# Kernel tuning notes

Measured on AMD Instinct MI355X. Metric: run time of the kernel, lower is better.

Reference implementation:

```python
import jax, jax.numpy as jnp
import numpy as np

T, E, D, F, K, CAP = 4096, 8, 1024, 4096, 2, 1024


def setup_inputs() -> dict:
    key = jax.random.key(0)
    ks = jax.random.split(key, 4)
    x = jax.random.normal(ks[0], (T, D), jnp.float32)
    # top-k routing: mask/weight consistent with a softmax router
    logits = jax.random.normal(ks[1], (T, E), jnp.float32)
    probs = jax.nn.softmax(logits, axis=-1)
    _, topi = jax.lax.top_k(probs, K)  # (T, K)
    route_mask = jnp.zeros((T, E), jnp.bool_).at[jnp.arange(T)[:, None], topi].set(True)
    route_weight = jnp.where(route_mask, probs, 0.0)
    # stacked expert MLP params (E leading axis, as ModuleGroup stacks them)
    w1 = jax.random.normal(ks[2], (E, D, F), jnp.float32) * 0.02
    b1 = jnp.zeros((E, F), jnp.float32)
    w2 = jax.random.normal(ks[3], (E, F, D), jnp.float32) * 0.02
    b2 = jnp.zeros((E, D), jnp.float32)
    return dict(x=x, route_mask=route_mask, route_weight=route_weight,
                w1=w1, b1=b1, w2=w2, b2=b2)


def _build_slots(mask_te, w_te, cap):
    # mask_te: (T,E) bool; w_te: (T,E) float (0 where unrouted)
    Tn, En = mask_te.shape
    m_et = mask_te.T                              # (E,T)
    w_et = jnp.where(m_et, w_te.T, -jnp.inf)      # unrouted -> -inf
    _, idx_top = jax.lax.top_k(w_et, cap)         # (E,C) token ids per slot
    slot = jnp.zeros((En, cap, Tn), w_te.dtype)
    slot = slot.at[jnp.arange(En)[:, None], jnp.arange(cap)[None, :], idx_top].set(1.0)
    slot = slot * m_et[:, None, :].astype(w_te.dtype)  # zero slots from -inf picks
    # NOTE: the original re-orders slots along C (a stable sort); the combine
    # einsum sums over C so the output is invariant to slot order -- skipped.
    return slot


def reference(x, route_mask, route_weight, w1, b1, w2, b2):
    w_te = jnp.where(route_mask, route_weight, 0.0)      # (T,E)
    slot = _build_slots(route_mask, w_te, CAP)           # (E,C,T) one-hot
    # dispatch: 'ect,t...->ec...'
    xs = jnp.einsum('ect,td->ecd', slot, x)              # (E,C,D)
    # expert compute (vmapped MLP over E)
    h = jax.nn.gelu(jnp.einsum('ecd,edf->ecf', xs, w1) + b1[:, None, :])
    out = jnp.einsum('ecf,efd->ecd', h, w2) + b2[:, None, :]
    # combine: 'ecf,ect,te->tf'
    y = jnp.einsum('ecd,ect,te->td', out, slot, w_te)    # (T,D)
    return y
```

## Files before the change

kernel.cpp:

```cpp
#include <hip/hip_runtime.h>
#include <hip/hip_bf16.h>
#include <stdint.h>

#define T_TOK 4096
#define E_EXP 8
#define D_DIM 1024
#define F_DIM 4096
#define K_TOP 2
#define CAPC  1024

typedef __attribute__((ext_vector_type(8))) short short8;
typedef __attribute__((ext_vector_type(4))) float f32x4;
typedef __attribute__((ext_vector_type(4))) unsigned short u16x4;
typedef __attribute__((ext_vector_type(8))) unsigned short u16x8;

static __device__ __forceinline__ unsigned short f2bf(float f) {
  union { float f; unsigned u; } v; v.f = f;
  unsigned r = v.u + 0x7fffu + ((v.u >> 16) & 1u);
  return (unsigned short)(r >> 16);
}

static __device__ __forceinline__ void gload_lds16(const void* g, void* l) {
  __builtin_amdgcn_global_load_lds(
      (const __attribute__((address_space(1))) unsigned int*)g,
      (__attribute__((address_space(3))) unsigned int*)l, 16, 0, 0);
}

__global__ void zero_int_kernel(int* p, int n) {
  int i = blockIdx.x * 256 + threadIdx.x;
  if (i < n) p[i] = 0;
}

#define PREP_SEL0   0
#define PREP_CVT0   8
#define PREP_TR0    4104
#define PREP_NBLK   12296

__global__ __launch_bounds__(256) void prep_kernel(
    const float* __restrict__ x,
    const float* __restrict__ rw,
    const float* __restrict__ w1,
    const float* __restrict__ w2,
    unsigned short* __restrict__ xb,
    unsigned short* __restrict__ w1t,
    unsigned short* __restrict__ w2t,
    int* __restrict__ sel_idx,
    int* __restrict__ inv_cnt,
    int* __restrict__ inv_ec,
    float* __restrict__ inv_w)
{
  __shared__ __align__(16) char smem[18560];
  __shared__ int sh_need;
  __shared__ unsigned sh_prefix;
  __shared__ int slot_ctr;
  const int bid = blockIdx.x;
  const int tid = threadIdx.x;

  if (bid >= PREP_TR0) {
    const int tb = bid - PREP_TR0;
    const float* inp; unsigned short* outp; int R, C, r0, c0;
    if (tb < 4096) {
      const int e = tb >> 9, ti = tb & 511;
      R = 1024; C = 4096;
      r0 = (ti & 7) * 128; c0 = (ti >> 3) * 64;
      inp = w1 + (size_t)e * R * C; outp = w1t + (size_t)e * R * C;
    } else {
      const int t2 = tb - 4096, e = t2 >> 9, ti = t2 & 511;
      R = 4096; C = 1024;
      r0 = (ti & 31) * 128; c0 = (ti >> 5) * 64;
      inp = w2 + (size_t)e * R * C; outp = w2t + (size_t)e * R * C;
    }
    unsigned short* tile = (unsigned short*)smem;
    const int q4 = (tid & 15) * 4, tr = tid >> 4;
    for (int rr = tr; rr < 128; rr += 16) {
      f32x4 v = *(const f32x4*)(inp + (size_t)(r0 + rr) * C + c0 + q4);
      unsigned* t32 = (unsigned*)(tile + rr * 66 + q4);
      t32[0] = (unsigned)f2bf(v.x) | ((unsigned)f2bf(v.y) << 16);
      t32[1] = (unsigned)f2bf(v.z) | ((unsigned)f2bf(v.w) << 16);
    }
    __syncthreads();
    const int l = tid & 15, ccb = tid >> 4;
#pragma unroll
    for (int it = 0; it < 4; ++it) {
      const int cc = ccb + it * 16;
      u16x8 o;
#pragma unroll
      for (int j = 0; j < 8; ++j) o[j] = tile[(l * 8 + j) * 66 + cc];
      *(u16x8*)(outp + (size_t)(c0 + cc) * R + r0 + l * 8) = o;
    }
    return;
  }

  if (bid >= PREP_CVT0) {
    const int i = (bid - PREP_CVT0) * 256 + tid;
    f32x4 v = ((const f32x4*)x)[i];
    u16x4 o = { f2bf(v.x), f2bf(v.y), f2bf(v.z), f2bf(v.w) };
    ((u16x4*)xb)[i] = o;
    return;
  }

  unsigned* keys = (unsigned*)smem;
  int* hist = (int*)(smem + 16384);
  int* scn  = (int*)(smem + 16384 + 1024);
  const int e = bid;
  for (int c = tid; c < CAPC; c += 256) sel_idx[e * CAPC + c] = -1;
#pragma unroll
  for (int j = 0; j < 16; ++j) {
    const int t = tid * 16 + j;
    const float w = rw[(size_t)t * E_EXP + e];
    keys[t] = (w > 0.f) ? __float_as_uint(w) : 0u;
  }
  if (tid == 0) slot_ctr = 0;

  int need = CAPC;
  unsigned prefix = 0;
  for (int shift = 24; shift >= 0; shift -= 8) {
    __syncthreads();
    hist[tid] = 0;
    __syncthreads();
#pragma unroll
    for (int j = 0; j < 16; ++j) {
      const unsigned k = keys[tid * 16 + j];
      const unsigned hi = (shift == 24) ? 0u : (k >> (shift + 8));
      if (hi == prefix) atomicAdd(&hist[(k >> shift) & 255u], 1);
    }
    __syncthreads();
    if (tid == 0) {
      int cum = 0, b;
      for (b = 255; b >= 0; --b) {
        cum += hist[b];
        if (cum >= need) break;
      }
      if (b < 0) b = 0;
      sh_need = need - (cum - hist[b]);
      sh_prefix = (prefix << 8) | (unsigned)b;
    }
    __syncthreads();
    need = sh_need;
    prefix = sh_prefix;
  }
  const unsigned thr = prefix;
  __syncthreads();

  int eqbits = 0, myeq = 0;
#pragma unroll
  for (int j = 0; j < 16; ++j) {
    const int t = tid * 16 + j;
    const unsigned k = keys[t];
    if (k > thr) {
      const int s = atomicAdd(&slot_ctr, 1);
      sel_idx[e * CAPC + s] = t;
      const int p = atomicAdd(&inv_cnt[t], 1);
      inv_ec[t * K_TOP + p] = e * CAPC + s;
      inv_w[t * K_TOP + p] = __uint_as_float(k);
    }
    if (thr > 0u && k == thr) { eqbits |= (1 << j); ++myeq; }
  }
  scn[tid] = myeq;
  __syncthreads();
  for (int d = 1; d < 256; d <<= 1) {
    const int v = scn[tid];
    const int a = (tid >= d) ? scn[tid - d] : 0;
    __syncthreads();
    scn[tid] = v + a;
    __syncthreads();
  }
  int r = scn[tid] - myeq;
  const int base = CAPC - need;
#pragma unroll
  for (int j = 0; j < 16; ++j) {
    if ((eqbits >> j) & 1) {
      if (r < need) {
        const int t = tid * 16 + j;
        const int s = base + r;
        sel_idx[e * CAPC + s] = t;
        const int p = atomicAdd(&inv_cnt[t], 1);
        inv_ec[t * K_TOP + p] = e * CAPC + s;
        inv_w[t * K_TOP + p] = __uint_as_float(thr);
      }
      ++r;
    }
  }
}


__global__ __launch_bounds__(256, 3) void gemm1_kernel(
    const unsigned short* __restrict__ xb,
    const int* __restrict__ sel_idx,
    const unsigned short* __restrict__ w1t,
    const float* __restrict__ b1,
    unsigned short* __restrict__ H)
{
  __shared__ __align__(16) unsigned short Asm[128 * 64];
  __shared__ __align__(16) unsigned short Bsm[128 * 64];
  const int e = blockIdx.z;
  const int m0 = blockIdx.y * 128;
  const int n0 = blockIdx.x * 128;
  const int tid = threadIdx.x;
  const int lane = tid & 63, wv = tid >> 6;
  const int wm = (wv >> 1) * 64, wn = (wv & 1) * 64;
  const int lrow = lane & 15, quad = lane >> 4;

  const int rbase = tid >> 3, seg = tid & 7;
  const int cs = seg ^ (rbase & 7);
  const unsigned short* gA[4];
  const unsigned short* gB[4];
  char* lA[4];
  char* lB[4];
  const unsigned short* w1e = w1t + (size_t)e * F_DIM * D_DIM;
#pragma unroll
  for (int it = 0; it < 4; ++it) {
    const int row = rbase + it * 32;
    int t = sel_idx[e * CAPC + m0 + row];
    if (t < 0) t = 0;
    gA[it] = xb + (size_t)t * D_DIM + cs * 8;
    gB[it] = w1e + (size_t)(n0 + row) * D_DIM + cs * 8;
    lA[it] = (char*)Asm + it * 4096 + wv * 1024;
    lB[it] = (char*)Bsm + it * 4096 + wv * 1024;
  }

  f32x4 acc[4][4];
#pragma unroll
  for (int a = 0; a < 4; ++a)
#pragma unroll
    for (int b = 0; b < 4; ++b) acc[a][b] = (f32x4){0.f, 0.f, 0.f, 0.f};

  const int sw = lrow & 7;
  for (int k0 = 0; k0 < D_DIM; k0 += 64) {
#pragma unroll
    for (int it = 0; it < 4; ++it) { gload_lds16(gA[it], lA[it]); gA[it] += 64; }
#pragma unroll
    for (int it = 0; it < 4; ++it) { gload_lds16(gB[it], lB[it]); gB[it] += 64; }
    __syncthreads();
#pragma unroll
    for (int h = 0; h < 2; ++h) {
      short8 af[4], bf[4];
#pragma unroll
      for (int mt = 0; mt < 4; ++mt)
        af[mt] = *(const short8*)(Asm + (wm + mt * 16 + lrow) * 64 +
                                  (((h << 2) + quad) ^ sw) * 8);
#pragma unroll
      for (int nt = 0; nt < 4; ++nt)
        bf[nt] = *(const short8*)(Bsm + (wn + nt * 16 + lrow) * 64 +
                                  (((h << 2) + quad) ^ sw) * 8);
#pragma unroll
      for (int mt = 0; mt < 4; ++mt)
#pragma unroll
        for (int nt = 0; nt < 4; ++nt)
          acc[mt][nt] = __builtin_amdgcn_mfma_f32_16x16x32_bf16(
              af[mt], bf[nt], acc[mt][nt], 0, 0, 0);
    }
    __syncthreads();
  }

  const float* b1e = b1 + e * F_DIM;
#pragma unroll
  for (int nt = 0; nt < 4; ++nt) {
    const int col = n0 + wn + nt * 16 + lrow;
    const float bias = b1e[col];
#pragma unroll
    for (int mt = 0; mt < 4; ++mt) {
      const int rowb = m0 + wm + mt * 16 + quad * 4;
#pragma unroll
      for (int i = 0; i < 4; ++i) {
        float v = acc[mt][nt][i] + bias;
        float u = 0.7978845608028654f * (v + 0.044715f * v * v * v);
        float th = 1.f - 2.f / (1.f + __expf(2.f * u));
        float hv = 0.5f * v * (1.f + th);
        H[((size_t)e * CAPC + rowb + i) * F_DIM + col] = f2bf(hv);
      }
    }
  }
}

__global__ __launch_bounds__(256, 3) void gemm2_kernel(
    const unsigned short* __restrict__ H,
    const unsigned short* __restrict__ w2t,
    const float* __restrict__ b2,
    float* __restrict__ P)
{
  __shared__ __align__(16) unsigned short Asm[128 * 64];
  __shared__ __align__(16) unsigned short Bsm[128 * 64];
  const int e = blockIdx.z & 7;
  const int ks = blockIdx.z >> 3;
  const int m0 = blockIdx.y * 128;
  const int n0 = blockIdx.x * 128;
  const int kbase = ks * (F_DIM / 2);
  const int tid = threadIdx.x;
  const int lane = tid & 63, wv = tid >> 6;
  const int wm = (wv >> 1) * 64, wn = (wv & 1) * 64;
  const int lrow = lane & 15, quad = lane >> 4;

  const int rbase = tid >> 3, seg = tid & 7;
  const int cs = seg ^ (rbase & 7);
  const unsigned short* gA[4];
  const unsigned short* gB[4];
  char* lA[4];
  char* lB[4];
  const unsigned short* He = H + (size_t)e * CAPC * F_DIM;
  const unsigned short* w2e = w2t + (size_t)e * D_DIM * F_DIM;
#pragma unroll
  for (int it = 0; it < 4; ++it) {
    const int row = rbase + it * 32;
    gA[it] = He + (size_t)(m0 + row) * F_DIM + kbase + cs * 8;
    gB[it] = w2e + (size_t)(n0 + row) * F_DIM + kbase + cs * 8;
    lA[it] = (char*)Asm + it * 4096 + wv * 1024;
    lB[it] = (char*)Bsm + it * 4096 + wv * 1024;
  }

  f32x4 acc[4][4];
#pragma unroll
  for (int a = 0; a < 4; ++a)
#pragma unroll
    for (int b = 0; b < 4; ++b) acc[a][b] = (f32x4){0.f, 0.f, 0.f, 0.f};

  const int sw = lrow & 7;
  for (int k0 = 0; k0 < F_DIM / 2; k0 += 64) {
#pragma unroll
    for (int it = 0; it < 4; ++it) { gload_lds16(gA[it], lA[it]); gA[it] += 64; }
#pragma unroll
    for (int it = 0; it < 4; ++it) { gload_lds16(gB[it], lB[it]); gB[it] += 64; }
    __syncthreads();
#pragma unroll
    for (int h = 0; h < 2; ++h) {
      short8 af[4], bf[4];
#pragma unroll
      for (int mt = 0; mt < 4; ++mt)
        af[mt] = *(const short8*)(Asm + (wm + mt * 16 + lrow) * 64 +
                                  (((h << 2) + quad) ^ sw) * 8);
#pragma unroll
      for (int nt = 0; nt < 4; ++nt)
        bf[nt] = *(const short8*)(Bsm + (wn + nt * 16 + lrow) * 64 +
                                  (((h << 2) + quad) ^ sw) * 8);
#pragma unroll
      for (int mt = 0; mt < 4; ++mt)
#pragma unroll
        for (int nt = 0; nt < 4; ++nt)
          acc[mt][nt] = __builtin_amdgcn_mfma_f32_16x16x32_bf16(
              af[mt], bf[nt], acc[mt][nt], 0, 0, 0);
    }
    __syncthreads();
  }

  const float* b2e = b2 + e * D_DIM;
  float* Pk = P + (size_t)ks * E_EXP * CAPC * D_DIM;
#pragma unroll
  for (int nt = 0; nt < 4; ++nt) {
    const int col = n0 + wn + nt * 16 + lrow;
    const float bias = (ks == 0) ? b2e[col] : 0.f;
#pragma unroll
    for (int mt = 0; mt < 4; ++mt) {
      const int rowb = m0 + wm + mt * 16 + quad * 4;
#pragma unroll
      for (int i = 0; i < 4; ++i) {
        Pk[((size_t)e * CAPC + rowb + i) * D_DIM + col] = acc[mt][nt][i] + bias;
      }
    }
  }
}

__global__ __launch_bounds__(256) void combine_kernel(
    const float* __restrict__ P, const int* __restrict__ inv_cnt,
    const int* __restrict__ inv_ec, const float* __restrict__ inv_w,
    float* __restrict__ y)
{
  const int t = blockIdx.x;
  const int cnt = inv_cnt[t];
  f32x4 s = {0.f, 0.f, 0.f, 0.f};
  const int d4 = threadIdx.x;
  const size_t half = (size_t)E_EXP * CAPC * D_DIM;
  for (int p = 0; p < cnt; ++p) {
    const int ec = inv_ec[t * K_TOP + p];
    const float w = inv_w[t * K_TOP + p];
    f32x4 v0 = ((const f32x4*)(P + (size_t)ec * D_DIM))[d4];
    f32x4 v1 = ((const f32x4*)(P + half + (size_t)ec * D_DIM))[d4];
    s += (v0 + v1) * w;
  }
  ((f32x4*)(y + (size_t)t * D_DIM))[d4] = s;
}

extern "C" void kernel_launch(void* const* d_in, const int* in_sizes, int n_in,
                              void* d_out, int out_size, void* d_ws, size_t ws_size,
                              hipStream_t stream) {
  (void)in_sizes; (void)n_in; (void)out_size; (void)ws_size;
  const float* x  = (const float*)d_in[0];
  const float* rw = (const float*)d_in[2];
  const float* w1 = (const float*)d_in[3];
  const float* b1 = (const float*)d_in[4];
  const float* w2 = (const float*)d_in[5];
  const float* b2 = (const float*)d_in[6];
  float* y = (float*)d_out;

  char* ws = (char*)d_ws;
  size_t off = 0;
  auto alloc = [&](size_t bytes) {
    void* p = ws + off;
    off += (bytes + 255) & ~(size_t)255;
    return p;
  };
  unsigned short* xb  = (unsigned short*)alloc((size_t)T_TOK * D_DIM * 2);
  unsigned short* w1t = (unsigned short*)alloc((size_t)E_EXP * F_DIM * D_DIM * 2);
  unsigned short* w2t = (unsigned short*)alloc((size_t)E_EXP * D_DIM * F_DIM * 2);
  unsigned short* H   = (unsigned short*)alloc((size_t)E_EXP * CAPC * F_DIM * 2);
  float* P            = (float*)alloc((size_t)2 * E_EXP * CAPC * D_DIM * 4);
  int* sel_idx        = (int*)alloc((size_t)E_EXP * CAPC * 4);
  int* inv_cnt        = (int*)alloc((size_t)T_TOK * 4);
  int* inv_ec         = (int*)alloc((size_t)T_TOK * K_TOP * 4);
  float* inv_w        = (float*)alloc((size_t)T_TOK * K_TOP * 4);

  zero_int_kernel<<<(T_TOK + 255) / 256, 256, 0, stream>>>(inv_cnt, T_TOK);

  prep_kernel<<<PREP_NBLK, 256, 0, stream>>>(
      x, rw, w1, w2, xb, w1t, w2t, sel_idx, inv_cnt, inv_ec, inv_w);

  gemm1_kernel<<<dim3(F_DIM / 128, CAPC / 128, E_EXP), 256, 0, stream>>>(
      xb, sel_idx, w1t, b1, H);
  gemm2_kernel<<<dim3(D_DIM / 128, CAPC / 128, E_EXP * 2), 256, 0, stream>>>(
      H, w2t, b2, P);

  combine_kernel<<<T_TOK, 256, 0, stream>>>(P, inv_cnt, inv_ec, inv_w, y);
}
```

Measured before the change: 534.4 us.

## Fuse combine into gemm2 epilogue via atomics and replace radix select with bitonic sort

The combine kernel and the fp32 partial-sum buffer P are removed. gemm2 now scatters weighted results directly into y with atomicAdd, after y is zeroed by a memset. The radix top-k selection is replaced by compaction plus an optional bitonic sort that only runs when more than CAP tokens route to an expert. GELU is rewritten as v*sigmoid(...) using a fast reciprocal. The atomics make the summation order nondeterministic and add atomic traffic to y in exchange for skipping the P write and re-read.

```diff
diff --git a/kernel.cpp b/kernel.cpp
--- a/kernel.cpp
+++ b/kernel.cpp
@@ -24,11 +24,6 @@
   __builtin_amdgcn_global_load_lds(
       (const __attribute__((address_space(1))) unsigned int*)g,
       (__attribute__((address_space(3))) unsigned int*)l, 16, 0, 0);
-}
-
-__global__ void zero_int_kernel(int* p, int n) {
-  int i = blockIdx.x * 256 + threadIdx.x;
-  if (i < n) p[i] = 0;
 }
 
 #define PREP_SEL0   0
@@ -45,14 +40,10 @@
     unsigned short* __restrict__ w1t,
     unsigned short* __restrict__ w2t,
     int* __restrict__ sel_idx,
-    int* __restrict__ inv_cnt,
-    int* __restrict__ inv_ec,
-    float* __restrict__ inv_w)
+    float* __restrict__ sel_w)
 {
-  __shared__ __align__(16) char smem[18560];
-  __shared__ int sh_need;
-  __shared__ unsigned sh_prefix;
-  __shared__ int slot_ctr;
+  __shared__ __align__(16) char smem[32768];
+  __shared__ int cnt_s;
   const int bid = blockIdx.x;
   const int tid = threadIdx.x;
 
@@ -99,87 +90,46 @@
     return;
   }
 
-  unsigned* keys = (unsigned*)smem;
-  int* hist = (int*)(smem + 16384);
-  int* scn  = (int*)(smem + 16384 + 1024);
+  unsigned long long* keys = (unsigned long long*)smem;
   const int e = bid;
   for (int c = tid; c < CAPC; c += 256) sel_idx[e * CAPC + c] = -1;
+  if (tid == 0) cnt_s = 0;
+  __syncthreads();
 #pragma unroll
   for (int j = 0; j < 16; ++j) {
     const int t = tid * 16 + j;
     const float w = rw[(size_t)t * E_EXP + e];
-    keys[t] = (w > 0.f) ? __float_as_uint(w) : 0u;
-  }
-  if (tid == 0) slot_ctr = 0;
-
-  int need = CAPC;
-  unsigned prefix = 0;
-  for (int shift = 24; shift >= 0; shift -= 8) {
-    __syncthreads();
-    hist[tid] = 0;
-    __syncthreads();
-#pragma unroll
-    for (int j = 0; j < 16; ++j) {
-      const unsigned k = keys[tid * 16 + j];
-      const unsigned hi = (shift == 24) ? 0u : (k >> (shift + 8));
-      if (hi == prefix) atomicAdd(&hist[(k >> shift) & 255u], 1);
-    }
-    __syncthreads();
-    if (tid == 0) {
-      int cum = 0, b;
-      for (b = 255; b >= 0; --b) {
-        cum += hist[b];
-        if (cum >= need) break;
+    if (w > 0.f) {
+      const int p = atomicAdd(&cnt_s, 1);
+      keys[p] = (((unsigned long long)__float_as_uint(w)) << 32)
+                | (unsigned)(4095 - t);
+    }
+  }
+  __syncthreads();
+  const int count = cnt_s;
+  if (count > CAPC) {
+    const int n = (count <= 2048) ? 2048 : 4096;
+    for (int i = count + tid; i < n; i += 256) keys[i] = 0ull;
+    for (int k = 2; k <= n; k <<= 1) {
+      for (int j = k >> 1; j > 0; j >>= 1) {
+        __syncthreads();
+        for (int i = tid; i < n; i += 256) {
+          const int ixj = i ^ j;
+          if (ixj > i) {
+            const unsigned long long a = keys[i], b = keys[ixj];
+            const bool swp = ((i & k) == 0) ? (a < b) : (a > b);
+            if (swp) { keys[i] = b; keys[ixj] = a; }
+          }
+        }
       }
-      if (b < 0) b = 0;
-      sh_need = need - (cum - hist[b]);
-      sh_prefix = (prefix << 8) | (unsigned)b;
-    }
-    __syncthreads();
-    need = sh_need;
-    prefix = sh_prefix;
-  }
-  const unsigned thr = prefix;
-  __syncthreads();
-
-  int eqbits = 0, myeq = 0;
-#pragma unroll
-  for (int j = 0; j < 16; ++j) {
-    const int t = tid * 16 + j;
-    const unsigned k = keys[t];
-    if (k > thr) {
-      const int s = atomicAdd(&slot_ctr, 1);
-      sel_idx[e * CAPC + s] = t;
-      const int p = atomicAdd(&inv_cnt[t], 1);
-      inv_ec[t * K_TOP + p] = e * CAPC + s;
-      inv_w[t * K_TOP + p] = __uint_as_float(k);
-    }
-    if (thr > 0u && k == thr) { eqbits |= (1 << j); ++myeq; }
-  }
-  scn[tid] = myeq;
-  __syncthreads();
-  for (int d = 1; d < 256; d <<= 1) {
-    const int v = scn[tid];
-    const int a = (tid >= d) ? scn[tid - d] : 0;
-    __syncthreads();
-    scn[tid] = v + a;
-    __syncthreads();
-  }
-  int r = scn[tid] - myeq;
-  const int base = CAPC - need;
-#pragma unroll
-  for (int j = 0; j < 16; ++j) {
-    if ((eqbits >> j) & 1) {
-      if (r < need) {
-        const int t = tid * 16 + j;
-        const int s = base + r;
-        sel_idx[e * CAPC + s] = t;
-        const int p = atomicAdd(&inv_cnt[t], 1);
-        inv_ec[t * K_TOP + p] = e * CAPC + s;
-        inv_w[t * K_TOP + p] = __uint_as_float(thr);
-      }
-      ++r;
-    }
+    }
+    __syncthreads();
+  }
+  const int nout = (count < CAPC) ? count : CAPC;
+  for (int c = tid; c < nout; c += 256) {
+    const unsigned long long k = keys[c];
+    sel_idx[e * CAPC + c] = 4095 - (int)(k & 0xffffffffu);
+    sel_w[e * CAPC + c] = __uint_as_float((unsigned)(k >> 32));
   }
 }
 
@@ -253,6 +203,8 @@
     __syncthreads();
   }
 
+  const float gk0 = -1.5957691216057308f;
+  const float gk1 = -0.07135486f;
   const float* b1e = b1 + e * F_DIM;
 #pragma unroll
   for (int nt = 0; nt < 4; ++nt) {
@@ -263,10 +215,9 @@
       const int rowb = m0 + wm + mt * 16 + quad * 4;
 #pragma unroll
       for (int i = 0; i < 4; ++i) {
-        float v = acc[mt][nt][i] + bias;
-        float u = 0.7978845608028654f * (v + 0.044715f * v * v * v);
-        float th = 1.f - 2.f / (1.f + __expf(2.f * u));
-        float hv = 0.5f * v * (1.f + th);
+        const float v = acc[mt][nt][i] + bias;
+        const float q = v * fmaf(gk1, v * v, gk0);
+        const float hv = v * __builtin_amdgcn_rcpf(1.f + __expf(q));
         H[((size_t)e * CAPC + rowb + i) * F_DIM + col] = f2bf(hv);
       }
     }
@@ -277,10 +228,14 @@
     const unsigned short* __restrict__ H,
     const unsigned short* __restrict__ w2t,
     const float* __restrict__ b2,
-    float* __restrict__ P)
+    const int* __restrict__ sel_idx,
+    const float* __restrict__ sel_w,
+    float* __restrict__ y)
 {
   __shared__ __align__(16) unsigned short Asm[128 * 64];
   __shared__ __align__(16) unsigned short Bsm[128 * 64];
+  __shared__ int rt[128];
+  __shared__ float rww[128];
   const int e = blockIdx.z & 7;
   const int ks = blockIdx.z >> 3;
   const int m0 = blockIdx.y * 128;
@@ -291,6 +246,11 @@
   const int wm = (wv >> 1) * 64, wn = (wv & 1) * 64;
   const int lrow = lane & 15, quad = lane >> 4;
 
+  if (tid < 128) {
+    rt[tid] = sel_idx[e * CAPC + m0 + tid];
+    rww[tid] = sel_w[e * CAPC + m0 + tid];
+  }
+
   const int rbase = tid >> 3, seg = tid & 7;
   const int cs = seg ^ (rbase & 7);
   const unsigned short* gA[4];
@@ -343,40 +303,23 @@
   }
 
   const float* b2e = b2 + e * D_DIM;
-  float* Pk = P + (size_t)ks * E_EXP * CAPC * D_DIM;
 #pragma unroll
   for (int nt = 0; nt < 4; ++nt) {
     const int col = n0 + wn + nt * 16 + lrow;
     const float bias = (ks == 0) ? b2e[col] : 0.f;
 #pragma unroll
     for (int mt = 0; mt < 4; ++mt) {
-      const int rowb = m0 + wm + mt * 16 + quad * 4;
+      const int rowb = wm + mt * 16 + quad * 4;
 #pragma unroll
       for (int i = 0; i < 4; ++i) {
-        Pk[((size_t)e * CAPC + rowb + i) * D_DIM + col] = acc[mt][nt][i] + bias;
+        const int row = rowb + i;
+        const int t = rt[row];
+        if (t >= 0)
+          atomicAdd(&y[(size_t)t * D_DIM + col],
+                    rww[row] * (acc[mt][nt][i] + bias));
       }
     }
   }
-}
-
-__global__ __launch_bounds__(256) void combine_kernel(
-    const float* __restrict__ P, const int* __restrict__ inv_cnt,
-    const int* __restrict__ inv_ec, const float* __restrict__ inv_w,
-    float* __restrict__ y)
-{
-  const int t = blockIdx.x;
-  const int cnt = inv_cnt[t];
-  f32x4 s = {0.f, 0.f, 0.f, 0.f};
-  const int d4 = threadIdx.x;
-  const size_t half = (size_t)E_EXP * CAPC * D_DIM;
-  for (int p = 0; p < cnt; ++p) {
-    const int ec = inv_ec[t * K_TOP + p];
-    const float w = inv_w[t * K_TOP + p];
-    f32x4 v0 = ((const f32x4*)(P + (size_t)ec * D_DIM))[d4];
-    f32x4 v1 = ((const f32x4*)(P + half + (size_t)ec * D_DIM))[d4];
-    s += (v0 + v1) * w;
-  }
-  ((f32x4*)(y + (size_t)t * D_DIM))[d4] = s;
 }
 
 extern "C" void kernel_launch(void* const* d_in, const int* in_sizes, int n_in,
@@ -402,21 +345,16 @@
   unsigned short* w1t = (unsigned short*)alloc((size_t)E_EXP * F_DIM * D_DIM * 2);
   unsigned short* w2t = (unsigned short*)alloc((size_t)E_EXP * D_DIM * F_DIM * 2);
   unsigned short* H   = (unsigned short*)alloc((size_t)E_EXP * CAPC * F_DIM * 2);
-  float* P            = (float*)alloc((size_t)2 * E_EXP * CAPC * D_DIM * 4);
   int* sel_idx        = (int*)alloc((size_t)E_EXP * CAPC * 4);
-  int* inv_cnt        = (int*)alloc((size_t)T_TOK * 4);
-  int* inv_ec         = (int*)alloc((size_t)T_TOK * K_TOP * 4);
-  float* inv_w        = (float*)alloc((size_t)T_TOK * K_TOP * 4);
-
-  zero_int_kernel<<<(T_TOK + 255) / 256, 256, 0, stream>>>(inv_cnt, T_TOK);
+  float* sel_w        = (float*)alloc((size_t)E_EXP * CAPC * 4);
+
+  hipMemsetAsync(y, 0, (size_t)T_TOK * D_DIM * 4, stream);
 
   prep_kernel<<<PREP_NBLK, 256, 0, stream>>>(
-      x, rw, w1, w2, xb, w1t, w2t, sel_idx, inv_cnt, inv_ec, inv_w);
+      x, rw, w1, w2, xb, w1t, w2t, sel_idx, sel_w);
 
   gemm1_kernel<<<dim3(F_DIM / 128, CAPC / 128, E_EXP), 256, 0, stream>>>(
       xb, sel_idx, w1t, b1, H);
   gemm2_kernel<<<dim3(D_DIM / 128, CAPC / 128, E_EXP * 2), 256, 0, stream>>>(
-      H, w2t, b2, P);
-
-  combine_kernel<<<T_TOK, 256, 0, stream>>>(P, inv_cnt, inv_ec, inv_w, y);
-}
+      H, w2t, b2, sel_idx, sel_w, y);
+}
```

New measurement: 563.4 us. 5.4% more time.
